# Optimization experiments

Measured on AMD Instinct MI355X. Metric: run time of the kernel, lower is better.

The kernel has to match this reference:

```python
import jax, jax.numpy as jnp
import numpy as np

MARGIN = 0.3  # init kwarg, mode='norm'


def _pairwise_dist(X):
    # squared euclidean distances, then safe sqrt (matches euc_dist(X.t()).sqrt())
    sq = jnp.sum(X * X, axis=1)                      # [n]
    d2 = sq[:, None] + sq[None, :] - 2.0 * (X @ X.T)  # [n, n]
    d2 = jnp.maximum(d2, 0.0)
    # safe sqrt: avoid inf derivative at 0 (diagonal); forward value identical
    return jnp.where(d2 > 0.0, jnp.sqrt(jnp.where(d2 > 0.0, d2, 1.0)), 0.0)


def setup_inputs() -> dict:
    key = jax.random.key(0)
    kx, ky = jax.random.split(key)
    X = jax.random.normal(kx, (4096, 2048), dtype=jnp.float32)
    Y = jax.random.randint(ky, (4096,), 0, 128, dtype=jnp.int64)
    return {"X": X, "Y": Y}


def reference(X, Y):
    dist = _pairwise_dist(X)                         # [n, n]
    mask = Y[:, None] == Y[None, :]                  # same-identity mask [n, n]
    inf = jnp.array(jnp.inf, dtype=dist.dtype)
    # hardest positive per anchor: max over same-label entries
    dist_ap = jnp.max(jnp.where(mask, dist, -inf), axis=1)  # [n]
    # hardest negative per anchor: min over different-label entries
    dist_an = jnp.min(jnp.where(mask, inf, dist), axis=1)   # [n]
    # mode == 'norm': mean hinge
    return jnp.mean(jnp.maximum(dist_ap - dist_an + MARGIN, 0.0))
```

## Files before the change

### kernel.cpp

```cpp
#include <hip/hip_runtime.h>
#include <hip/hip_bf16.h>
#include <hip/hip_fp8.h>

typedef __attribute__((ext_vector_type(4))) int i32x4;
typedef __attribute__((ext_vector_type(8))) int i32x8;
typedef __attribute__((ext_vector_type(16))) float f32x16;

#define MARGIN 0.3f
#define BIGF 3.0e38f

__device__ __forceinline__ void gl2lds16(const void* g, void* l) {
    __builtin_amdgcn_global_load_lds(
        (const __attribute__((address_space(1))) void*)g,
        (__attribute__((address_space(3))) void*)l,
        16, 0, 0);
}

__global__ __launch_bounds__(256) void convert_norm_kernel(
    const float* __restrict__ X, unsigned char* __restrict__ Xq,
    float* __restrict__ nrm, unsigned* __restrict__ ap,
    unsigned* __restrict__ an, unsigned* __restrict__ cnt, int K) {
    const int wave = threadIdx.x >> 6, lane = threadIdx.x & 63;
    const int row = blockIdx.x * 4 + wave;
    const float* xr = X + (size_t)row * K;
    unsigned char* xqr = Xq + (size_t)row * K;
    float s = 0.0f;
    for (int c = lane * 8; c < K; c += 64 * 8) {
        float4 v0 = *(const float4*)(xr + c);
        float4 v1 = *(const float4*)(xr + c + 4);
        float f[8] = {v0.x, v0.y, v0.z, v0.w, v1.x, v1.y, v1.z, v1.w};
        union { unsigned char b[8]; uint2 u; } p;
#pragma unroll
        for (int i = 0; i < 8; i++) {
            __hip_fp8_e4m3 q(f[i]);
            p.b[i] = q.__x;
            float d = (float)q;
            s += d * d;
        }
        *(uint2*)(xqr + c) = p.u;
    }
    for (int off = 32; off > 0; off >>= 1) s += __shfl_xor(s, off, 64);
    if (lane == 0) {
        nrm[row] = s;
        ap[row] = 0u;
        an[row] = 0x7F800000u;
        if (row == 0) *cnt = 0u;
    }
}

__global__ __launch_bounds__(256) void gemm_reduce_kernel(
    const unsigned char* __restrict__ Xq, const float* __restrict__ nrm,
    const int* __restrict__ Y, unsigned* __restrict__ ap,
    unsigned* __restrict__ an, unsigned* __restrict__ cnt,
    float* __restrict__ out, int N, int K) {
    __shared__ __align__(16) unsigned char sA[64 * 128];
    __shared__ __align__(16) unsigned char sB[128 * 128];
    __shared__ int sYr[64], sYc[128];
    __shared__ float sNr[64], sNc[128];
    __shared__ float redmax[4][64], redmin[4][64];
    __shared__ float lsum[4];
    __shared__ unsigned s_done;

    const int tid = threadIdx.x;
    const int wave = tid >> 6;
    const int lane = tid & 63;
    const int m = lane & 31;
    const int h = lane >> 5;

    int j = 0;
    {
        const int b = blockIdx.x;
        while ((j + 1) * (j + 2) <= b) j++;
    }
    const int r = blockIdx.x - j * (j + 1);
    const int rowBase = r * 64;
    const int colBase = j * 128;

    if (tid < 64) {
        sYr[tid] = Y[rowBase + tid];
        sNr[tid] = nrm[rowBase + tid];
    } else if (tid < 192) {
        int t = tid - 64;
        sYc[t] = Y[colBase + t];
        sNc[t] = nrm[colBase + t];
    }

    f32x16 acc[2];
#pragma unroll
    for (int si = 0; si < 2; si++)
#pragma unroll
        for (int rr = 0; rr < 16; rr++) acc[si][rr] = 0.0f;

    const int rsub = lane >> 3;
    const int jchunk = (lane & 7) ^ rsub;
    const unsigned char* gA = Xq + (size_t)(rowBase + wave * 16 + rsub) * K + jchunk * 16;
    const unsigned char* gB = Xq + (size_t)(colBase + wave * 32 + rsub) * K + jchunk * 16;
    unsigned char* lA = sA + wave * 2048;
    unsigned char* lB = sB + wave * 4096;
    const size_t g8 = (size_t)8 * K;

    const int e = m & 7;
    const int nit = K >> 7;

    for (int it = 0; it < nit; it++) {
        const size_t go = (size_t)it * 128;
        gl2lds16(gA + go, lA);
        gl2lds16(gA + go + g8, lA + 1024);
        gl2lds16(gB + go, lB);
        gl2lds16(gB + go + g8, lB + 1024);
        gl2lds16(gB + go + 2 * g8, lB + 2048);
        gl2lds16(gB + go + 3 * g8, lB + 3072);
        __syncthreads();

#pragma unroll
        for (int s = 0; s < 2; s++) {
            const int c0 = s * 4 + h * 2;
            i32x8 af[2], bf;
#pragma unroll
            for (int si = 0; si < 2; si++) {
                const unsigned char* base = sA + (si * 32 + m) * 128;
                i32x4 lo = *(const i32x4*)(base + ((c0 ^ e) * 16));
                i32x4 hi = *(const i32x4*)(base + (((c0 + 1) ^ e) * 16));
                af[si] = __builtin_shufflevector(lo, hi, 0, 1, 2, 3, 4, 5, 6, 7);
            }
            {
                const unsigned char* base = sB + (wave * 32 + m) * 128;
                i32x4 lo = *(const i32x4*)(base + ((c0 ^ e) * 16));
                i32x4 hi = *(const i32x4*)(base + (((c0 + 1) ^ e) * 16));
                bf = __builtin_shufflevector(lo, hi, 0, 1, 2, 3, 4, 5, 6, 7);
            }
#pragma unroll
            for (int si = 0; si < 2; si++)
                acc[si] = __builtin_amdgcn_mfma_scale_f32_32x32x64_f8f6f4(
                    af[si], bf, acc[si], 0 , 0 ,
                    0, 127 , 0, 127 );
        }
        __syncthreads();
    }

    const int col = wave * 32 + m;
    const int yc = sYc[col];
    const float ncol = sNc[col];
    float cmx = -1.0f, cmn = BIGF;

#pragma unroll
    for (int si = 0; si < 2; si++)
#pragma unroll
        for (int reg = 0; reg < 16; reg++) {
            const int row64 = si * 32 + (reg & 3) + 8 * (reg >> 2) + 4 * h;
            float d2 = sNr[row64] + ncol - 2.0f * acc[si][reg];
            float d = sqrtf(fmaxf(d2, 0.0f));
            bool same = (sYr[row64] == yc);
            float dp = same ? d : -1.0f;
            float dn = same ? BIGF : d;
            cmx = fmaxf(cmx, dp);
            cmn = fminf(cmn, dn);
            float mx = dp, mn = dn;
            for (int off = 1; off < 32; off <<= 1) {
                mx = fmaxf(mx, __shfl_xor(mx, off, 64));
                mn = fminf(mn, __shfl_xor(mn, off, 64));
            }
            if (m == 0) {
                redmax[wave][row64] = mx;
                redmin[wave][row64] = mn;
            }
        }

    cmx = fmaxf(cmx, __shfl_xor(cmx, 32, 64));
    cmn = fminf(cmn, __shfl_xor(cmn, 32, 64));
    if (h == 0) {
        atomicMax(&ap[colBase + col], __float_as_uint(fmaxf(cmx, 0.0f)));
        atomicMin(&an[colBase + col], __float_as_uint(cmn));
    }
    __syncthreads();

    if (tid < 64) {
        float mx = fmaxf(fmaxf(redmax[0][tid], redmax[1][tid]),
                         fmaxf(redmax[2][tid], redmax[3][tid]));
        float mn = fminf(fminf(redmin[0][tid], redmin[1][tid]),
                         fminf(redmin[2][tid], redmin[3][tid]));
        atomicMax(&ap[rowBase + tid], __float_as_uint(fmaxf(mx, 0.0f)));
        atomicMin(&an[rowBase + tid], __float_as_uint(mn));
    }

    __syncthreads();
    if (tid == 0) {
        __threadfence();
        s_done = atomicAdd(cnt, 1u);
    }
    __syncthreads();
    if (s_done == gridDim.x - 1) {
        __threadfence();
        float s = 0.0f;
        for (int i = tid; i < N; i += 256) {
            unsigned ua = __hip_atomic_load(&ap[i], __ATOMIC_RELAXED,
                                            __HIP_MEMORY_SCOPE_AGENT);
            unsigned ub = __hip_atomic_load(&an[i], __ATOMIC_RELAXED,
                                            __HIP_MEMORY_SCOPE_AGENT);
            s += fmaxf(__uint_as_float(ua) - __uint_as_float(ub) + MARGIN, 0.0f);
        }
        for (int off = 32; off > 0; off >>= 1) s += __shfl_xor(s, off, 64);
        if (lane == 0) lsum[wave] = s;
        __syncthreads();
        if (tid == 0)
            out[0] = (lsum[0] + lsum[1] + lsum[2] + lsum[3]) / (float)N;
    }
}

extern "C" void kernel_launch(void* const* d_in, const int* in_sizes, int n_in,
                              void* d_out, int out_size, void* d_ws, size_t ws_size,
                              hipStream_t stream) {
    const float* X = (const float*)d_in[0];
    const int* Y = (const int*)d_in[1];
    float* out = (float*)d_out;
    const int N = in_sizes[1];
    const int K = in_sizes[0] / N;

    char* ws = (char*)d_ws;
    unsigned char* Xq = (unsigned char*)ws;
    float* nrm = (float*)(ws + (size_t)N * K);
    unsigned* ap = (unsigned*)((char*)nrm + (size_t)N * 4);
    unsigned* an = (unsigned*)((char*)ap + (size_t)N * 4);
    unsigned* cnt = (unsigned*)((char*)an + (size_t)N * 4);

    convert_norm_kernel<<<N / 4, 256, 0, stream>>>(X, Xq, nrm, ap, an, cnt, K);
    const int NB = N / 128;
    const int nblocks = NB * (NB + 1);
    gemm_reduce_kernel<<<nblocks, 256, 0, stream>>>(Xq, nrm, Y, ap, an, cnt,
                                                    out, N, K);
}
```

Measured before the change: 147.8 us.

## Use single-wave 64x64 triangular tiles with per-wave 2x2 MFMA blocking

Replaces the four-wave 64x128 block tiling with a one-wave block that owns a 64x64 upper-triangular tile and computes a 2x2 grid of 32x32 MFMA accumulators. Block-wide barriers become wave-local waitcnt instructions, and the LDS reduction buffers are dropped in favour of direct atomics and global loads of labels and norms. The aim is to remove barrier overhead and exploit symmetry more finely. In exchange there are many more small blocks with less parallelism per block for latency hiding, more atomics per tile, and twice the number of done-counter increments.

```diff
diff --git a/kernel.cpp b/kernel.cpp
--- a/kernel.cpp
+++ b/kernel.cpp
@@ -48,55 +48,36 @@
     }
 }
 
-__global__ __launch_bounds__(256) void gemm_reduce_kernel(
+__global__ __launch_bounds__(64) void gemm_reduce_kernel(
     const unsigned char* __restrict__ Xq, const float* __restrict__ nrm,
     const int* __restrict__ Y, unsigned* __restrict__ ap,
     unsigned* __restrict__ an, unsigned* __restrict__ cnt,
     float* __restrict__ out, int N, int K) {
     __shared__ __align__(16) unsigned char sA[64 * 128];
-    __shared__ __align__(16) unsigned char sB[128 * 128];
-    __shared__ int sYr[64], sYc[128];
-    __shared__ float sNr[64], sNc[128];
-    __shared__ float redmax[4][64], redmin[4][64];
-    __shared__ float lsum[4];
-    __shared__ unsigned s_done;
-
-    const int tid = threadIdx.x;
-    const int wave = tid >> 6;
-    const int lane = tid & 63;
+    __shared__ __align__(16) unsigned char sB[64 * 128];
+
+    const int lane = threadIdx.x;
     const int m = lane & 31;
     const int h = lane >> 5;
 
-    int j = 0;
-    {
-        const int b = blockIdx.x;
-        while ((j + 1) * (j + 2) <= b) j++;
-    }
-    const int r = blockIdx.x - j * (j + 1);
-    const int rowBase = r * 64;
-    const int colBase = j * 128;
-
-    if (tid < 64) {
-        sYr[tid] = Y[rowBase + tid];
-        sNr[tid] = nrm[rowBase + tid];
-    } else if (tid < 192) {
-        int t = tid - 64;
-        sYc[t] = Y[colBase + t];
-        sNc[t] = nrm[colBase + t];
-    }
-
-    f32x16 acc[2];
+    const int NB = N >> 6;
+    int ib = 0, rem = blockIdx.x;
+    while (rem >= NB - ib) { rem -= NB - ib; ib++; }
+    const int rowB = ib * 64;
+    const int colB = (ib + rem) * 64;
+
+    f32x16 acc[2][2];
 #pragma unroll
     for (int si = 0; si < 2; si++)
 #pragma unroll
-        for (int rr = 0; rr < 16; rr++) acc[si][rr] = 0.0f;
+        for (int sj = 0; sj < 2; sj++)
+#pragma unroll
+            for (int rr = 0; rr < 16; rr++) acc[si][sj][rr] = 0.0f;
 
     const int rsub = lane >> 3;
     const int jchunk = (lane & 7) ^ rsub;
-    const unsigned char* gA = Xq + (size_t)(rowBase + wave * 16 + rsub) * K + jchunk * 16;
-    const unsigned char* gB = Xq + (size_t)(colBase + wave * 32 + rsub) * K + jchunk * 16;
-    unsigned char* lA = sA + wave * 2048;
-    unsigned char* lB = sB + wave * 4096;
+    const unsigned char* gA = Xq + (size_t)(rowB + rsub) * K + jchunk * 16;
+    const unsigned char* gB = Xq + (size_t)(colB + rsub) * K + jchunk * 16;
     const size_t g8 = (size_t)8 * K;
 
     const int e = m & 7;
@@ -104,18 +85,18 @@
 
     for (int it = 0; it < nit; it++) {
         const size_t go = (size_t)it * 128;
-        gl2lds16(gA + go, lA);
-        gl2lds16(gA + go + g8, lA + 1024);
-        gl2lds16(gB + go, lB);
-        gl2lds16(gB + go + g8, lB + 1024);
-        gl2lds16(gB + go + 2 * g8, lB + 2048);
-        gl2lds16(gB + go + 3 * g8, lB + 3072);
-        __syncthreads();
+#pragma unroll
+        for (int gi = 0; gi < 8; gi++)
+            gl2lds16(gA + go + gi * g8, sA + gi * 1024);
+#pragma unroll
+        for (int gi = 0; gi < 8; gi++)
+            gl2lds16(gB + go + gi * g8, sB + gi * 1024);
+        asm volatile("s_waitcnt vmcnt(0)" ::: "memory");
 
 #pragma unroll
         for (int s = 0; s < 2; s++) {
             const int c0 = s * 4 + h * 2;
-            i32x8 af[2], bf;
+            i32x8 af[2], bf[2];
 #pragma unroll
             for (int si = 0; si < 2; si++) {
                 const unsigned char* base = sA + (si * 32 + m) * 128;
@@ -123,76 +104,86 @@
                 i32x4 hi = *(const i32x4*)(base + (((c0 + 1) ^ e) * 16));
                 af[si] = __builtin_shufflevector(lo, hi, 0, 1, 2, 3, 4, 5, 6, 7);
             }
-            {
-                const unsigned char* base = sB + (wave * 32 + m) * 128;
+#pragma unroll
+            for (int sj = 0; sj < 2; sj++) {
+                const unsigned char* base = sB + (sj * 32 + m) * 128;
                 i32x4 lo = *(const i32x4*)(base + ((c0 ^ e) * 16));
                 i32x4 hi = *(const i32x4*)(base + (((c0 + 1) ^ e) * 16));
-                bf = __builtin_shufflevector(lo, hi, 0, 1, 2, 3, 4, 5, 6, 7);
+                bf[sj] = __builtin_shufflevector(lo, hi, 0, 1, 2, 3, 4, 5, 6, 7);
             }
 #pragma unroll
             for (int si = 0; si < 2; si++)
-                acc[si] = __builtin_amdgcn_mfma_scale_f32_32x32x64_f8f6f4(
-                    af[si], bf, acc[si], 0 , 0 ,
-                    0, 127 , 0, 127 );
-        }
-        __syncthreads();
-    }
-
-    const int col = wave * 32 + m;
-    const int yc = sYc[col];
-    const float ncol = sNc[col];
-    float cmx = -1.0f, cmn = BIGF;
+#pragma unroll
+                for (int sj = 0; sj < 2; sj++)
+                    acc[si][sj] = __builtin_amdgcn_mfma_scale_f32_32x32x64_f8f6f4(
+                        af[si], bf[sj], acc[si][sj], 0 ,
+                        0 , 0, 127 ,
+                        0, 127 );
+        }
+        asm volatile("s_waitcnt lgkmcnt(0)" ::: "memory");
+    }
+
+    int yc[2]; float ncv[2];
+#pragma unroll
+    for (int sj = 0; sj < 2; sj++) {
+        yc[sj] = Y[colB + sj * 32 + m];
+        ncv[sj] = nrm[colB + sj * 32 + m];
+    }
+
+    float cmx[2], cmn[2];
+    cmx[0] = cmx[1] = -1.0f;
+    cmn[0] = cmn[1] = BIGF;
 
 #pragma unroll
     for (int si = 0; si < 2; si++)
 #pragma unroll
         for (int reg = 0; reg < 16; reg++) {
-            const int row64 = si * 32 + (reg & 3) + 8 * (reg >> 2) + 4 * h;
-            float d2 = sNr[row64] + ncol - 2.0f * acc[si][reg];
-            float d = sqrtf(fmaxf(d2, 0.0f));
-            bool same = (sYr[row64] == yc);
-            float dp = same ? d : -1.0f;
-            float dn = same ? BIGF : d;
-            cmx = fmaxf(cmx, dp);
-            cmn = fminf(cmn, dn);
-            float mx = dp, mn = dn;
+            const int r64 = si * 32 + (reg & 3) + 8 * (reg >> 2) + 4 * h;
+            const int yr = Y[rowB + r64];
+            const float nr = nrm[rowB + r64];
+            float dp = -1.0f, dn = BIGF;
+#pragma unroll
+            for (int sj = 0; sj < 2; sj++) {
+                float d2 = nr + ncv[sj] - 2.0f * acc[si][sj][reg];
+                float d = sqrtf(fmaxf(d2, 0.0f));
+                bool same = (yr == yc[sj]);
+                float p = same ? d : -1.0f;
+                float n = same ? BIGF : d;
+                dp = fmaxf(dp, p);
+                dn = fminf(dn, n);
+                cmx[sj] = fmaxf(cmx[sj], p);
+                cmn[sj] = fminf(cmn[sj], n);
+            }
             for (int off = 1; off < 32; off <<= 1) {
-                mx = fmaxf(mx, __shfl_xor(mx, off, 64));
-                mn = fminf(mn, __shfl_xor(mn, off, 64));
+                dp = fmaxf(dp, __shfl_xor(dp, off, 64));
+                dn = fminf(dn, __shfl_xor(dn, off, 64));
             }
             if (m == 0) {
-                redmax[wave][row64] = mx;
-                redmin[wave][row64] = mn;
-            }
-        }
-
-    cmx = fmaxf(cmx, __shfl_xor(cmx, 32, 64));
-    cmn = fminf(cmn, __shfl_xor(cmn, 32, 64));
-    if (h == 0) {
-        atomicMax(&ap[colBase + col], __float_as_uint(fmaxf(cmx, 0.0f)));
-        atomicMin(&an[colBase + col], __float_as_uint(cmn));
-    }
-    __syncthreads();
-
-    if (tid < 64) {
-        float mx = fmaxf(fmaxf(redmax[0][tid], redmax[1][tid]),
-                         fmaxf(redmax[2][tid], redmax[3][tid]));
-        float mn = fminf(fminf(redmin[0][tid], redmin[1][tid]),
-                         fminf(redmin[2][tid], redmin[3][tid]));
-        atomicMax(&ap[rowBase + tid], __float_as_uint(fmaxf(mx, 0.0f)));
-        atomicMin(&an[rowBase + tid], __float_as_uint(mn));
-    }
-
-    __syncthreads();
-    if (tid == 0) {
+                atomicMax(&ap[rowB + r64], __float_as_uint(fmaxf(dp, 0.0f)));
+                atomicMin(&an[rowB + r64], __float_as_uint(dn));
+            }
+        }
+
+#pragma unroll
+    for (int sj = 0; sj < 2; sj++) {
+        float mx = fmaxf(cmx[sj], __shfl_xor(cmx[sj], 32, 64));
+        float mn = fminf(cmn[sj], __shfl_xor(cmn[sj], 32, 64));
+        if (h == 0) {
+            atomicMax(&ap[colB + sj * 32 + m], __float_as_uint(fmaxf(mx, 0.0f)));
+            atomicMin(&an[colB + sj * 32 + m], __float_as_uint(mn));
+        }
+    }
+
+    unsigned mydone = 0;
+    if (lane == 0) {
         __threadfence();
-        s_done = atomicAdd(cnt, 1u);
-    }
-    __syncthreads();
-    if (s_done == gridDim.x - 1) {
+        mydone = atomicAdd(cnt, 1u);
+    }
+    const unsigned done = __shfl(mydone, 0, 64);
+    if (done == gridDim.x - 1) {
         __threadfence();
         float s = 0.0f;
-        for (int i = tid; i < N; i += 256) {
+        for (int i = lane; i < N; i += 64) {
             unsigned ua = __hip_atomic_load(&ap[i], __ATOMIC_RELAXED,
                                             __HIP_MEMORY_SCOPE_AGENT);
             unsigned ub = __hip_atomic_load(&an[i], __ATOMIC_RELAXED,
@@ -200,10 +191,7 @@
             s += fmaxf(__uint_as_float(ua) - __uint_as_float(ub) + MARGIN, 0.0f);
         }
         for (int off = 32; off > 0; off >>= 1) s += __shfl_xor(s, off, 64);
-        if (lane == 0) lsum[wave] = s;
-        __syncthreads();
-        if (tid == 0)
-            out[0] = (lsum[0] + lsum[1] + lsum[2] + lsum[3]) / (float)N;
+        if (lane == 0) out[0] = s / (float)N;
     }
 }
 
@@ -224,8 +212,8 @@
     unsigned* cnt = (unsigned*)((char*)an + (size_t)N * 4);
 
     convert_norm_kernel<<<N / 4, 256, 0, stream>>>(X, Xq, nrm, ap, an, cnt, K);
-    const int NB = N / 128;
-    const int nblocks = NB * (NB + 1);
-    gemm_reduce_kernel<<<nblocks, 256, 0, stream>>>(Xq, nrm, Y, ap, an, cnt,
-                                                    out, N, K);
-}
+    const int NB = N / 64;
+    const int ntiles = NB * (NB + 1) / 2;
+    gemm_reduce_kernel<<<ntiles, 64, 0, stream>>>(Xq, nrm, Y, ap, an, cnt,
+                                                  out, N, K);
+}
```

Measured after the change: 193.5 us. 30.9% more time.

## Prefetch next K-tile into registers to overlap global loads with MFMA

Applied to the files above, without the earlier changes.

Replaces direct global-to-LDS loads with register-staged loads. The next K tile is fetched into registers while MFMAs run on the current tile, then written to LDS between barriers. This is meant to hide global memory latency behind compute in the main loop. In exchange it uses more VGPRs and adds extra LDS write instructions, and it still keeps two barriers per iteration with a single LDS buffer.

```diff
diff --git a/kernel.cpp b/kernel.cpp
--- a/kernel.cpp
+++ b/kernel.cpp
@@ -9,12 +9,7 @@
 #define MARGIN 0.3f
 #define BIGF 3.0e38f
 
-__device__ __forceinline__ void gl2lds16(const void* g, void* l) {
-    __builtin_amdgcn_global_load_lds(
-        (const __attribute__((address_space(1))) void*)g,
-        (__attribute__((address_space(3))) void*)l,
-        16, 0, 0);
-}
+#define BAR_LGKM() asm volatile("s_waitcnt lgkmcnt(0)\n\ts_barrier" ::: "memory")
 
 __global__ __launch_bounds__(256) void convert_norm_kernel(
     const float* __restrict__ X, unsigned char* __restrict__ Xq,
@@ -95,22 +90,41 @@
     const int jchunk = (lane & 7) ^ rsub;
     const unsigned char* gA = Xq + (size_t)(rowBase + wave * 16 + rsub) * K + jchunk * 16;
     const unsigned char* gB = Xq + (size_t)(colBase + wave * 32 + rsub) * K + jchunk * 16;
-    unsigned char* lA = sA + wave * 2048;
-    unsigned char* lB = sB + wave * 4096;
+    unsigned char* lA = sA + wave * 2048 + lane * 16;
+    unsigned char* lB = sB + wave * 4096 + lane * 16;
     const size_t g8 = (size_t)8 * K;
 
     const int e = m & 7;
     const int nit = K >> 7;
 
+    uint4 pa[2], pb[4];
+#define LOADT(it)                                                   \
+    {                                                               \
+        const size_t go = (size_t)(it) * 128;                       \
+        pa[0] = *(const uint4*)(gA + go);                           \
+        pa[1] = *(const uint4*)(gA + go + g8);                      \
+        pb[0] = *(const uint4*)(gB + go);                           \
+        pb[1] = *(const uint4*)(gB + go + g8);                      \
+        pb[2] = *(const uint4*)(gB + go + 2 * g8);                  \
+        pb[3] = *(const uint4*)(gB + go + 3 * g8);                  \
+    }
+#define WRITET()                                                    \
+    {                                                               \
+        *(uint4*)(lA) = pa[0];                                      \
+        *(uint4*)(lA + 1024) = pa[1];                               \
+        *(uint4*)(lB) = pb[0];                                      \
+        *(uint4*)(lB + 1024) = pb[1];                               \
+        *(uint4*)(lB + 2048) = pb[2];                               \
+        *(uint4*)(lB + 3072) = pb[3];                               \
+    }
+
+    LOADT(0);
+    WRITET();
+    BAR_LGKM();
+
     for (int it = 0; it < nit; it++) {
-        const size_t go = (size_t)it * 128;
-        gl2lds16(gA + go, lA);
-        gl2lds16(gA + go + g8, lA + 1024);
-        gl2lds16(gB + go, lB);
-        gl2lds16(gB + go + g8, lB + 1024);
-        gl2lds16(gB + go + 2 * g8, lB + 2048);
-        gl2lds16(gB + go + 3 * g8, lB + 3072);
-        __syncthreads();
+        const bool more = (it + 1 < nit);
+        if (more) LOADT(it + 1);
 
 #pragma unroll
         for (int s = 0; s < 2; s++) {
@@ -135,7 +149,12 @@
                     af[si], bf, acc[si], 0 , 0 ,
                     0, 127 , 0, 127 );
         }
-        __syncthreads();
+
+        if (more) {
+            BAR_LGKM();
+            WRITET();
+            BAR_LGKM();
+        }
     }
 
     const int col = wave * 32 + m;
```

Result: slower. 251.1 us (+69.9%).

## Use full 128x128 tiles over the whole grid instead of symmetric triangular tiles

Applied to the files above, without the earlier changes.

Replaces the triangular schedule of 64x128 tiles, which used symmetry to update both row and column reductions, with a full N×N grid of 128x128 tiles arranged as 2x2 waves. Each tile only reduces per row, which removes the column atomics and the triangular index search. Each block now reuses more data per LDS load and issues four MFMAs per k-step, at the price of computing roughly twice the total GEMM work. It also hardcodes blockIdx>>5, which assumes NB=32.

```diff
diff --git a/kernel.cpp b/kernel.cpp
--- a/kernel.cpp
+++ b/kernel.cpp
@@ -48,15 +48,15 @@
     }
 }
 
-__global__ __launch_bounds__(256) void gemm_reduce_kernel(
+__global__ __launch_bounds__(256, 4) void gemm_reduce_kernel(
     const unsigned char* __restrict__ Xq, const float* __restrict__ nrm,
     const int* __restrict__ Y, unsigned* __restrict__ ap,
     unsigned* __restrict__ an, unsigned* __restrict__ cnt,
     float* __restrict__ out, int N, int K) {
-    __shared__ __align__(16) unsigned char sA[64 * 128];
+    __shared__ __align__(16) unsigned char sA[128 * 128];
     __shared__ __align__(16) unsigned char sB[128 * 128];
-    __shared__ int sYr[64], sYc[128];
-    __shared__ float sNr[64], sNc[128];
+    __shared__ int sYr[128], sYc[128];
+    __shared__ float sNr[128], sNc[128];
     __shared__ float redmax[4][64], redmin[4][64];
     __shared__ float lsum[4];
     __shared__ unsigned s_done;
@@ -66,36 +66,35 @@
     const int lane = tid & 63;
     const int m = lane & 31;
     const int h = lane >> 5;
-
-    int j = 0;
-    {
-        const int b = blockIdx.x;
-        while ((j + 1) * (j + 2) <= b) j++;
-    }
-    const int r = blockIdx.x - j * (j + 1);
-    const int rowBase = r * 64;
-    const int colBase = j * 128;
-
-    if (tid < 64) {
+    const int wr = wave >> 1;
+    const int wc = wave & 1;
+
+    const int NB = N >> 7;
+    const int rowBase = (blockIdx.x >> 5) * 128;
+    const int colBase = (blockIdx.x & (NB - 1)) * 128;
+
+    if (tid < 128) {
         sYr[tid] = Y[rowBase + tid];
         sNr[tid] = nrm[rowBase + tid];
-    } else if (tid < 192) {
-        int t = tid - 64;
+    } else {
+        int t = tid - 128;
         sYc[t] = Y[colBase + t];
         sNc[t] = nrm[colBase + t];
     }
 
-    f32x16 acc[2];
+    f32x16 acc[2][2];
 #pragma unroll
     for (int si = 0; si < 2; si++)
 #pragma unroll
-        for (int rr = 0; rr < 16; rr++) acc[si][rr] = 0.0f;
+        for (int sj = 0; sj < 2; sj++)
+#pragma unroll
+            for (int rr = 0; rr < 16; rr++) acc[si][sj][rr] = 0.0f;
 
     const int rsub = lane >> 3;
     const int jchunk = (lane & 7) ^ rsub;
-    const unsigned char* gA = Xq + (size_t)(rowBase + wave * 16 + rsub) * K + jchunk * 16;
+    const unsigned char* gA = Xq + (size_t)(rowBase + wave * 32 + rsub) * K + jchunk * 16;
     const unsigned char* gB = Xq + (size_t)(colBase + wave * 32 + rsub) * K + jchunk * 16;
-    unsigned char* lA = sA + wave * 2048;
+    unsigned char* lA = sA + wave * 4096;
     unsigned char* lB = sB + wave * 4096;
     const size_t g8 = (size_t)8 * K;
 
@@ -104,81 +103,76 @@
 
     for (int it = 0; it < nit; it++) {
         const size_t go = (size_t)it * 128;
-        gl2lds16(gA + go, lA);
-        gl2lds16(gA + go + g8, lA + 1024);
-        gl2lds16(gB + go, lB);
-        gl2lds16(gB + go + g8, lB + 1024);
-        gl2lds16(gB + go + 2 * g8, lB + 2048);
-        gl2lds16(gB + go + 3 * g8, lB + 3072);
+#pragma unroll
+        for (int g = 0; g < 4; g++) {
+            gl2lds16(gA + go + g * g8, lA + g * 1024);
+            gl2lds16(gB + go + g * g8, lB + g * 1024);
+        }
         __syncthreads();
 
 #pragma unroll
         for (int s = 0; s < 2; s++) {
             const int c0 = s * 4 + h * 2;
-            i32x8 af[2], bf;
+            i32x8 af[2], bf[2];
 #pragma unroll
             for (int si = 0; si < 2; si++) {
-                const unsigned char* base = sA + (si * 32 + m) * 128;
+                const unsigned char* base = sA + (wr * 64 + si * 32 + m) * 128;
                 i32x4 lo = *(const i32x4*)(base + ((c0 ^ e) * 16));
                 i32x4 hi = *(const i32x4*)(base + (((c0 + 1) ^ e) * 16));
                 af[si] = __builtin_shufflevector(lo, hi, 0, 1, 2, 3, 4, 5, 6, 7);
             }
-            {
-                const unsigned char* base = sB + (wave * 32 + m) * 128;
+#pragma unroll
+            for (int sj = 0; sj < 2; sj++) {
+                const unsigned char* base = sB + (wc * 64 + sj * 32 + m) * 128;
                 i32x4 lo = *(const i32x4*)(base + ((c0 ^ e) * 16));
                 i32x4 hi = *(const i32x4*)(base + (((c0 + 1) ^ e) * 16));
-                bf = __builtin_shufflevector(lo, hi, 0, 1, 2, 3, 4, 5, 6, 7);
+                bf[sj] = __builtin_shufflevector(lo, hi, 0, 1, 2, 3, 4, 5, 6, 7);
             }
 #pragma unroll
             for (int si = 0; si < 2; si++)
-                acc[si] = __builtin_amdgcn_mfma_scale_f32_32x32x64_f8f6f4(
-                    af[si], bf, acc[si], 0 , 0 ,
-                    0, 127 , 0, 127 );
+#pragma unroll
+                for (int sj = 0; sj < 2; sj++)
+                    acc[si][sj] = __builtin_amdgcn_mfma_scale_f32_32x32x64_f8f6f4(
+                        af[si], bf[sj], acc[si][sj], 0 ,
+                        0 , 0, 127 ,
+                        0, 127 );
         }
         __syncthreads();
     }
-
-    const int col = wave * 32 + m;
-    const int yc = sYc[col];
-    const float ncol = sNc[col];
-    float cmx = -1.0f, cmn = BIGF;
 
 #pragma unroll
     for (int si = 0; si < 2; si++)
 #pragma unroll
         for (int reg = 0; reg < 16; reg++) {
             const int row64 = si * 32 + (reg & 3) + 8 * (reg >> 2) + 4 * h;
-            float d2 = sNr[row64] + ncol - 2.0f * acc[si][reg];
-            float d = sqrtf(fmaxf(d2, 0.0f));
-            bool same = (sYr[row64] == yc);
-            float dp = same ? d : -1.0f;
-            float dn = same ? BIGF : d;
-            cmx = fmaxf(cmx, dp);
-            cmn = fminf(cmn, dn);
-            float mx = dp, mn = dn;
+            const int rIdx = wr * 64 + row64;
+            const int yr = sYr[rIdx];
+            const float nr = sNr[rIdx];
+            float dp = -1.0f, dn = BIGF;
+#pragma unroll
+            for (int sj = 0; sj < 2; sj++) {
+                const int cIdx = wc * 64 + sj * 32 + m;
+                float d2 = nr + sNc[cIdx] - 2.0f * acc[si][sj][reg];
+                float d = sqrtf(fmaxf(d2, 0.0f));
+                bool same = (yr == sYc[cIdx]);
+                dp = fmaxf(dp, same ? d : -1.0f);
+                dn = fminf(dn, same ? BIGF : d);
+            }
             for (int off = 1; off < 32; off <<= 1) {
-                mx = fmaxf(mx, __shfl_xor(mx, off, 64));
-                mn = fminf(mn, __shfl_xor(mn, off, 64));
+                dp = fmaxf(dp, __shfl_xor(dp, off, 64));
+                dn = fminf(dn, __shfl_xor(dn, off, 64));
             }
             if (m == 0) {
-                redmax[wave][row64] = mx;
-                redmin[wave][row64] = mn;
-            }
-        }
-
-    cmx = fmaxf(cmx, __shfl_xor(cmx, 32, 64));
-    cmn = fminf(cmn, __shfl_xor(cmn, 32, 64));
-    if (h == 0) {
-        atomicMax(&ap[colBase + col], __float_as_uint(fmaxf(cmx, 0.0f)));
-        atomicMin(&an[colBase + col], __float_as_uint(cmn));
-    }
+                redmax[wave][row64] = dp;
+                redmin[wave][row64] = dn;
+            }
+        }
     __syncthreads();
 
-    if (tid < 64) {
-        float mx = fmaxf(fmaxf(redmax[0][tid], redmax[1][tid]),
-                         fmaxf(redmax[2][tid], redmax[3][tid]));
-        float mn = fminf(fminf(redmin[0][tid], redmin[1][tid]),
-                         fminf(redmin[2][tid], redmin[3][tid]));
+    if (tid < 128) {
+        const int wr2 = tid >> 6, r64 = tid & 63;
+        float mx = fmaxf(redmax[wr2 * 2][r64], redmax[wr2 * 2 + 1][r64]);
+        float mn = fminf(redmin[wr2 * 2][r64], redmin[wr2 * 2 + 1][r64]);
         atomicMax(&ap[rowBase + tid], __float_as_uint(fmaxf(mx, 0.0f)));
         atomicMin(&an[rowBase + tid], __float_as_uint(mn));
     }
@@ -225,7 +219,6 @@
 
     convert_norm_kernel<<<N / 4, 256, 0, stream>>>(X, Xq, nrm, ap, an, cnt, K);
     const int NB = N / 128;
-    const int nblocks = NB * (NB + 1);
-    gemm_reduce_kernel<<<nblocks, 256, 0, stream>>>(Xq, nrm, Y, ap, an, cnt,
+    gemm_reduce_kernel<<<NB * NB, 256, 0, stream>>>(Xq, nrm, Y, ap, an, cnt,
                                                     out, N, K);
 }
```

Result: faster. 133.2 us (-9.9%).
